# Optimization experiments

Measured on AMD Instinct MI355X. Metric: run time of the kernel, lower is better.

The kernel has to match this reference:

```python
import jax, jax.numpy as jnp
import numpy as np

TAU = 2.0       # LIF time constant
VTH = 1.0       # V_THRESHOLD
ALPHA = 2.0     # ATan surrogate alpha (spikingjelly default)
SCALE = 0.125

@jax.custom_vjp
def spike(x):
    # Heaviside spike with ATan surrogate gradient
    return (x >= 0.0).astype(x.dtype)

def _spike_fwd(x):
    return (x >= 0.0).astype(x.dtype), x

def _spike_bwd(x, g):
    sg = (ALPHA / 2.0) / (1.0 + (jnp.pi / 2.0 * ALPHA * x) ** 2)
    return (g * sg,)

spike.defvjp(_spike_fwd, _spike_bwd)

def lif(x_seq):
    # multi-step LIF: v += (x - v)/tau; spike; hard reset (v_reset=0, detach_reset)
    def step(v, x):
        v = v + (x - v) / TAU
        s = spike(v - VTH)
        v = v * (1.0 - jax.lax.stop_gradient(s))
        return v, s
    _, s = jax.lax.scan(step, jnp.zeros_like(x_seq[0]), x_seq)
    return s

def conn_lif(x_seq, y_seq):
    # connecting LIF: membrane charged by conv output + identity shortcut
    def step(v, xy):
        x, y = xy
        v = v + ((x + y) - v) / TAU
        s = spike(v - VTH)
        v = v * (1.0 - jax.lax.stop_gradient(s))
        return v, s
    _, s = jax.lax.scan(step, jnp.zeros_like(x_seq[0]), (x_seq, y_seq))
    return s

def conv1x1(x, W, b):
    # x: [T,B,C,N]; 1x1 Conv1d == channel GEMM
    return jnp.einsum('tbcn,oc->tbon', x, W) + b[None, None, :, None]

def setup_inputs() -> dict:
    key = jax.random.key(0)
    T, B, C, H, W = 4, 16, 512, 32, 32
    ks = jax.random.split(key, 5)
    wscale = 1.0 / np.sqrt(C)
    inp = {
        'x': jax.random.normal(ks[0], (T, B, C, H, W), jnp.float32),
        'Wq': jax.random.normal(ks[1], (C, C), jnp.float32) * wscale,
        'bq': jnp.zeros((C,), jnp.float32),
        'Wk': jax.random.normal(ks[2], (C, C), jnp.float32) * wscale,
        'bk': jnp.zeros((C,), jnp.float32),
        'Wv': jax.random.normal(ks[3], (C, C), jnp.float32) * wscale,
        'bv': jnp.zeros((C,), jnp.float32),
        'Wp': jax.random.normal(ks[4], (C, C), jnp.float32) * wscale,
        'bp': jnp.zeros((C,), jnp.float32),
        'num_heads': 8,
    }
    return inp

def reference(x, Wq, bq, Wk, bk, Wv, bv, Wp, bp, num_heads):
    T, B, C, H, W = x.shape
    N = H * W
    h = num_heads
    d = C // h
    qkv_x = x.reshape(T, B, C, N)

    def to_heads(s):  # [T,B,C,N] -> [T,B,h,N,d]
        return s.reshape(T, B, h, d, N).transpose(0, 1, 2, 4, 3)

    q = to_heads(lif(conv1x1(qkv_x, Wq, bq)))
    k = to_heads(lif(conv1x1(qkv_x, Wk, bk)))
    v = to_heads(lif(conv1x1(qkv_x, Wv, bv)))

    kv = jnp.einsum('tbhnd,tbhne->tbhde', k, v)            # K^T V: [T,B,h,d,d]
    out = jnp.einsum('tbhnd,tbhde->tbhne', q, kv) * SCALE  # Q @ (K^T V)
    out = out.transpose(0, 1, 2, 4, 3).reshape(T, B, C, N)
    out = lif(out)                                          # attn_sn
    out = conv1x1(out, Wp, bp).reshape(T, B, C, H, W)       # proj_reparam
    out = conn_lif(out, x)                                  # proj_sn(out, x)
    return out
```

## Files before the change

### kernel.cpp

```cpp
#include <hip/hip_runtime.h>

#define T_ 4
#define B_ 16
#define C_ 512
#define N_ 1024
#define H_ 8
#define D_ 64
#define SPK_ELEMS (33554432ull)

typedef _Float16 half8v __attribute__((ext_vector_type(8)));
typedef _Float16 half4v __attribute__((ext_vector_type(4)));
typedef float f32x4 __attribute__((ext_vector_type(4)));

#define KV_OFF_N  100663296ull
#define WB_OFF_N  109051904ull
#define XS_OFF_N  113246208ull

#define QKV_INV_SCALE (1.0f / 8388608.0f)
#define PROJ_INV_SCALE (1.0f / 4096.0f)

#define GLD16(gp, loff) \
  __builtin_amdgcn_global_load_lds( \
      (const __attribute__((address_space(1))) void*)(gp), \
      (__attribute__((address_space(3))) void*)(lds + (loff)), 16, 0, 0)

__global__ __launch_bounds__(256) void convert_w(
    const float* __restrict__ w0, const float* __restrict__ w1,
    const float* __restrict__ w2, const float* __restrict__ w3,
    _Float16* __restrict__ wb)
{
  int idx = blockIdx.x * 256 + threadIdx.x;
  int p = idx >> 18, rem = idx & 262143;
  const float* src = (p == 0) ? w0 : (p == 1) ? w1 : (p == 2) ? w2 : w3;
  float v = src[rem] * 4096.0f;
  _Float16 h1 = (_Float16)v;
  float r1 = v - (float)h1;
  _Float16 h2 = (_Float16)r1;
  size_t base = ((size_t)(p * 2)) << 18;
  wb[base + rem] = h1;
  wb[base + 262144 + rem] = h2;
}

__global__ __launch_bounds__(256) void convert_x(
    const float* __restrict__ x, _Float16* __restrict__ xs)
{
  __shared__ float tile[32][33];
  const int tb = blockIdx.z;
  const int c0 = blockIdx.y * 32, n0 = blockIdx.x * 32;
  const int tx = threadIdx.x, ty = threadIdx.y;
  const float* src = x + ((size_t)tb * C_ + c0) * N_ + n0;
#pragma unroll
  for (int k = 0; k < 4; ++k)
    tile[ty + 8 * k][tx] = src[(size_t)(ty + 8 * k) * N_ + tx];
  __syncthreads();
#pragma unroll
  for (int k = 0; k < 4; ++k) {
    int r = ty + 8 * k;
    float v = tile[tx][r] * 2048.0f;
    _Float16 h1 = (_Float16)v;
    float r1 = v - (float)h1;
    _Float16 h2 = (_Float16)r1;
    size_t o = ((size_t)tb * N_ + n0 + r) * C_ + c0 + tx;
    xs[o] = h1;
    xs[o + 33554432ull] = h2;
  }
}

__global__ __launch_bounds__(256) void qkv_mfma(
    const _Float16* __restrict__ wb, const _Float16* __restrict__ xs,
    const float* __restrict__ bq, const float* __restrict__ bk,
    const float* __restrict__ bv, unsigned char* __restrict__ spikes_base)
{
  __shared__ __align__(16) char lds[65536];
  const int tid = threadIdx.x;
  const int lane = tid & 63, wave = tid >> 6;
  const int ln15 = lane & 15, lq = lane >> 4;
  const int ot = blockIdx.x & 3, p = blockIdx.x >> 2;
  const int ntb = blockIdx.y, b = blockIdx.z;
  const int o0 = ot * 128, n0 = ntb * 32;

  const _Float16* gsrc[8];
#pragma unroll
  for (int i = 0; i < 8; ++i) {
    int u = i * 256 + tid;
    if (u < 1024) {
      int s = u >> 9, rem = u & 511;
      int row = rem >> 2, pc = rem & 3;
      int lc = pc ^ ((row >> 1) & 3);
      gsrc[i] = wb + (((size_t)(p * 2 + s)) << 18) + (size_t)(o0 + row) * C_ + lc * 8;
    } else {
      int v = u - 1024;
      int s = v >> 9, rem = v & 511;
      int t = rem >> 7, rem2 = rem & 127;
      int row = rem2 >> 2, pc = rem2 & 3;
      int lc = pc ^ ((row >> 1) & 3);
      gsrc[i] = xs + ((size_t)s * 33554432ull) +
                ((size_t)((t * B_ + b) * N_ + n0 + row)) * C_ + lc * 8;
    }
  }

  f32x4 acc[T_][2][2];
#pragma unroll
  for (int t = 0; t < T_; ++t)
#pragma unroll
    for (int mt = 0; mt < 2; ++mt)
#pragma unroll
      for (int nt = 0; nt < 2; ++nt)
        acc[t][mt][nt] = (f32x4){0.f, 0.f, 0.f, 0.f};

  int offA[2][2], offB[2][2];
#pragma unroll
  for (int s = 0; s < 2; ++s) {
#pragma unroll
    for (int mt = 0; mt < 2; ++mt) {
      int r = wave * 32 + mt * 16 + ln15;
      offA[s][mt] = s * 8192 + r * 64 + ((lq ^ ((r >> 1) & 3)) << 4);
    }
#pragma unroll
    for (int nt = 0; nt < 2; ++nt) {
      int n = nt * 16 + ln15;
      offB[s][nt] = 16384 + s * 8192 + n * 64 + ((lq ^ ((n >> 1) & 3)) << 4);
    }
  }

  auto compute = [&](int cur) {
    half8v wa[2][2];
#pragma unroll
    for (int s = 0; s < 2; ++s)
#pragma unroll
      for (int mt = 0; mt < 2; ++mt)
        wa[s][mt] = *(const half8v*)&lds[cur + offA[s][mt]];

    __builtin_amdgcn_s_setprio(1);
#pragma unroll
    for (int t = 0; t < T_; ++t) {
      half8v xb[2][2];
#pragma unroll
      for (int s = 0; s < 2; ++s)
#pragma unroll
        for (int nt = 0; nt < 2; ++nt)
          xb[s][nt] = *(const half8v*)&lds[cur + offB[s][nt] + t * 2048];
#pragma unroll
      for (int mt = 0; mt < 2; ++mt)
#pragma unroll
        for (int nt = 0; nt < 2; ++nt) {
          f32x4 a = acc[t][mt][nt];
          a = __builtin_amdgcn_mfma_f32_16x16x32_f16(wa[0][mt], xb[1][nt], a, 0, 0, 0);
          a = __builtin_amdgcn_mfma_f32_16x16x32_f16(wa[1][mt], xb[0][nt], a, 0, 0, 0);
          a = __builtin_amdgcn_mfma_f32_16x16x32_f16(wa[0][mt], xb[0][nt], a, 0, 0, 0);
          acc[t][mt][nt] = a;
        }
    }
    __builtin_amdgcn_s_setprio(0);
  };

#pragma unroll
  for (int i = 0; i < 8; ++i)
    GLD16(gsrc[i], i * 4096 + (tid & 192) * 16);
#pragma unroll
  for (int i = 0; i < 8; ++i) gsrc[i] += 32;

  for (int kk = 0; kk < 15; ++kk) {
    const int cur = (kk & 1) << 15;
    const int nxt = cur ^ 32768;
#pragma unroll
    for (int i = 0; i < 8; ++i)
      GLD16(gsrc[i], nxt + i * 4096 + (tid & 192) * 16);
#pragma unroll
    for (int i = 0; i < 8; ++i) gsrc[i] += 32;
    __builtin_amdgcn_sched_barrier(0);
    asm volatile("s_waitcnt vmcnt(8)" ::: "memory");
    __builtin_amdgcn_s_barrier();
    __builtin_amdgcn_sched_barrier(0);

    compute(cur);

    asm volatile("s_waitcnt lgkmcnt(0)" ::: "memory");
    __builtin_amdgcn_sched_barrier(0);
    __builtin_amdgcn_s_barrier();
  }
  asm volatile("s_waitcnt vmcnt(0)" ::: "memory");
  __builtin_amdgcn_s_barrier();
  __builtin_amdgcn_sched_barrier(0);
  compute(32768);

  const float* bias = (p == 0) ? bq : (p == 1) ? bk : bv;
  if (p == 0) {
    unsigned char* spq = spikes_base;
#pragma unroll
    for (int mt = 0; mt < 2; ++mt) {
      int obase = o0 + wave * 32 + mt * 16 + lq * 4;
      float b4[4] = {bias[obase], bias[obase + 1], bias[obase + 2], bias[obase + 3]};
#pragma unroll
      for (int nt = 0; nt < 2; ++nt) {
        int n = n0 + nt * 16 + ln15;
        float vm[4] = {0.f, 0.f, 0.f, 0.f};
#pragma unroll
        for (int t = 0; t < T_; ++t) {
          unsigned char sj[4];
#pragma unroll
          for (int r = 0; r < 4; ++r) {
            float y = acc[t][mt][nt][r] * QKV_INV_SCALE + b4[r];
            float v = vm[r] + (y - vm[r]) * 0.5f;
            bool s = (v >= 1.0f);
            sj[r] = s ? 1 : 0;
            vm[r] = s ? 0.f : v;
          }
          *(uchar4*)&spq[((size_t)(t * B_ + b) * N_ + n) * C_ + obase] =
              make_uchar4(sj[0], sj[1], sj[2], sj[3]);
        }
      }
    }
  } else {
    unsigned char* sp = spikes_base + (size_t)p * SPK_ELEMS;
#pragma unroll
    for (int mt = 0; mt < 2; ++mt)
#pragma unroll
      for (int r = 0; r < 4; ++r) {
        int o = o0 + wave * 32 + mt * 16 + lq * 4 + r;
        float bo = bias[o];
#pragma unroll
        for (int nt = 0; nt < 2; ++nt) {
          int n = n0 + nt * 16 + ln15;
          float vmem = 0.f;
#pragma unroll
          for (int t = 0; t < T_; ++t) {
            float y = acc[t][mt][nt][r] * QKV_INV_SCALE + bo;
            float v = vmem + (y - vmem) * 0.5f;
            bool s = (v >= 1.0f);
            sp[((size_t)(t * B_ + b) * C_ + o) * N_ + n] = s ? 1 : 0;
            vmem = s ? 0.f : v;
          }
        }
      }
  }
}

__global__ __launch_bounds__(256) void kv_f16(
    const unsigned char* __restrict__ sk, const unsigned char* __restrict__ sv,
    float* __restrict__ kvout)
{
  __shared__ _Float16 Kf[64 * 264];
  __shared__ _Float16 Vf[64 * 264];
  const int tid = threadIdx.x;
  const int lane = tid & 63, wave = tid >> 6;
  const int ln15 = lane & 15, lq = lane >> 4;
  const int h = blockIdx.x, b = blockIdx.y, t = blockIdx.z;

  const unsigned char* kb = sk + ((size_t)(t * B_ + b) * C_ + h * D_) * N_;
  const unsigned char* vb = sv + ((size_t)(t * B_ + b) * C_ + h * D_) * N_;

  f32x4 acc[4];
#pragma unroll
  for (int et = 0; et < 4; ++et) acc[et] = (f32x4){0.f, 0.f, 0.f, 0.f};

  const int row = tid >> 2, seg = (tid & 3) * 64;

  for (int nc = 0; nc < N_; nc += 256) {
    const unsigned char* kr = kb + (size_t)row * N_ + nc + seg;
    const unsigned char* vr = vb + (size_t)row * N_ + nc + seg;
#pragma unroll
    for (int j = 0; j < 16; ++j) {
      unsigned wk = *(const unsigned*)(kr + j * 4);
      unsigned lo = ((wk & 0xFFu) | ((wk & 0xFF00u) << 8)) * 0x3C00u;
      unsigned hi = (((wk >> 16) & 0xFFu) | ((wk >> 8) & 0xFF0000u)) * 0x3C00u;
      *(uint2*)&Kf[row * 264 + seg + j * 4] = make_uint2(lo, hi);
      unsigned wv = *(const unsigned*)(vr + j * 4);
      unsigned lo2 = ((wv & 0xFFu) | ((wv & 0xFF00u) << 8)) * 0x3C00u;
      unsigned hi2 = (((wv >> 16) & 0xFFu) | ((wv >> 8) & 0xFF0000u)) * 0x3C00u;
      *(uint2*)&Vf[row * 264 + seg + j * 4] = make_uint2(lo2, hi2);
    }
    __syncthreads();
#pragma unroll
    for (int ks = 0; ks < 8; ++ks) {
      half8v a = *(const half8v*)&Kf[(wave * 16 + ln15) * 264 + ks * 32 + lq * 8];
#pragma unroll
      for (int et = 0; et < 4; ++et) {
        half8v bf = *(const half8v*)&Vf[(et * 16 + ln15) * 264 + ks * 32 + lq * 8];
        acc[et] = __builtin_amdgcn_mfma_f32_16x16x32_f16(a, bf, acc[et], 0, 0, 0);
      }
    }
    __syncthreads();
  }

  float* o = kvout + ((size_t)(t * B_ + b) * H_ + h) * (D_ * D_);
#pragma unroll
  for (int et = 0; et < 4; ++et)
#pragma unroll
    for (int r = 0; r < 4; ++r) {
      int d = wave * 16 + lq * 4 + r;
      int e = et * 16 + ln15;
      o[d * D_ + e] = acc[et][r];
    }
}

__global__ __launch_bounds__(256) void attn_mfma(
    const unsigned char* __restrict__ sq2, const float* __restrict__ kv,
    unsigned short* __restrict__ sa)
{
  __shared__ _Float16 Qs[128 * 72];
  __shared__ _Float16 KVT[64 * 72];
  const int tid = threadIdx.x;
  const int lane = tid & 63, wave = tid >> 6;
  const int ln15 = lane & 15, lq = lane >> 4;
  const int n0 = blockIdx.x * 128;
  const int h = blockIdx.y, b = blockIdx.z;

  f32x4 vm[8];
#pragma unroll
  for (int nt = 0; nt < 8; ++nt) vm[nt] = (f32x4){0.f, 0.f, 0.f, 0.f};

  for (int t = 0; t < T_; ++t) {
    __syncthreads();
    const float* kvb = kv + ((size_t)(t * B_ + b) * H_ + h) * (D_ * D_);
#pragma unroll
    for (int l = 0; l < 16; ++l) {
      int idx = l * 256 + tid;
      int e = idx & 63, d = idx >> 6;
      KVT[e * 72 + d] = (_Float16)kvb[d * 64 + e];
    }
    const unsigned char* qb = sq2 + ((size_t)(t * B_ + b) * N_ + n0) * C_ + h * D_;
#pragma unroll
    for (int l = 0; l < 8; ++l) {
      int idx = l * 256 + tid;
      int n = idx >> 4, d4 = (idx & 15) * 4;
      uchar4 qu = *(const uchar4*)&qb[(size_t)n * C_ + d4];
      half4v hv;
      hv.x = qu.x ? (_Float16)1.0f : (_Float16)0.0f;
      hv.y = qu.y ? (_Float16)1.0f : (_Float16)0.0f;
      hv.z = qu.z ? (_Float16)1.0f : (_Float16)0.0f;
      hv.w = qu.w ? (_Float16)1.0f : (_Float16)0.0f;
      *(half4v*)&Qs[n * 72 + d4] = hv;
    }
    __syncthreads();

    half8v af[2];
#pragma unroll
    for (int kk = 0; kk < 2; ++kk)
      af[kk] = *(const half8v*)&KVT[(wave * 16 + ln15) * 72 + kk * 32 + lq * 8];

#pragma unroll
    for (int nt = 0; nt < 8; ++nt) {
      f32x4 a = (f32x4){0.f, 0.f, 0.f, 0.f};
#pragma unroll
      for (int kk = 0; kk < 2; ++kk) {
        half8v bf = *(const half8v*)&Qs[(nt * 16 + ln15) * 72 + kk * 32 + lq * 8];
        a = __builtin_amdgcn_mfma_f32_16x16x32_f16(af[kk], bf, a, 0, 0, 0);
      }
      unsigned short sj[4];
#pragma unroll
      for (int r = 0; r < 4; ++r) {
        float y = a[r] * 0.125f;
        float v = vm[nt][r] + (y - vm[nt][r]) * 0.5f;
        bool s = (v >= 1.0f);
        sj[r] = s ? 0x3C00 : 0;
        vm[nt][r] = s ? 0.f : v;
      }
      int n = n0 + nt * 16 + ln15;
      int c0 = h * D_ + wave * 16 + lq * 4;
      *(ushort4*)&sa[((size_t)(t * B_ + b) * N_ + n) * C_ + c0] =
          make_ushort4(sj[0], sj[1], sj[2], sj[3]);
    }
  }
}

__global__ __launch_bounds__(256) void proj_mfma(
    const _Float16* __restrict__ wb, const _Float16* __restrict__ sa,
    const float* __restrict__ bp, const float* __restrict__ x,
    float* __restrict__ out)
{
  __shared__ __align__(16) char lds[49152];
  const int tid = threadIdx.x;
  const int lane = tid & 63, wave = tid >> 6;
  const int ln15 = lane & 15, lq = lane >> 4;
  const int ot = blockIdx.x, ntb = blockIdx.y, b = blockIdx.z;
  const int o0 = ot * 128, n0 = ntb * 32;

  const _Float16* gsrc[6];
#pragma unroll
  for (int i = 0; i < 6; ++i) {
    int u = i * 256 + tid;
    if (u < 1024) {
      int s = u >> 9, rem = u & 511;
      int row = rem >> 2, pc = rem & 3;
      int lc = pc ^ ((row >> 1) & 3);
      gsrc[i] = wb + (((size_t)(3 * 2 + s)) << 18) + (size_t)(o0 + row) * C_ + lc * 8;
    } else {
      int v = u - 1024;
      int t = v >> 7, rem2 = v & 127;
      int row = rem2 >> 2, pc = rem2 & 3;
      int lc = pc ^ ((row >> 1) & 3);
      gsrc[i] = sa + ((size_t)((t * B_ + b) * N_ + n0 + row)) * C_ + lc * 8;
    }
  }

  f32x4 acc[T_][2][2];
#pragma unroll
  for (int t = 0; t < T_; ++t)
#pragma unroll
    for (int mt = 0; mt < 2; ++mt)
#pragma unroll
      for (int nt = 0; nt < 2; ++nt)
        acc[t][mt][nt] = (f32x4){0.f, 0.f, 0.f, 0.f};

  int offA[2][2], offB[2];
#pragma unroll
  for (int s = 0; s < 2; ++s)
#pragma unroll
    for (int mt = 0; mt < 2; ++mt) {
      int r = wave * 32 + mt * 16 + ln15;
      offA[s][mt] = s * 8192 + r * 64 + ((lq ^ ((r >> 1) & 3)) << 4);
    }
#pragma unroll
  for (int nt = 0; nt < 2; ++nt) {
    int n = nt * 16 + ln15;
    offB[nt] = 16384 + n * 64 + ((lq ^ ((n >> 1) & 3)) << 4);
  }

  auto compute = [&](int cur) {
    half8v wa[2][2];
#pragma unroll
    for (int s = 0; s < 2; ++s)
#pragma unroll
      for (int mt = 0; mt < 2; ++mt)
        wa[s][mt] = *(const half8v*)&lds[cur + offA[s][mt]];

    __builtin_amdgcn_s_setprio(1);
#pragma unroll
    for (int t = 0; t < T_; ++t) {
      half8v xb[2];
#pragma unroll
      for (int nt = 0; nt < 2; ++nt)
        xb[nt] = *(const half8v*)&lds[cur + offB[nt] + t * 2048];
#pragma unroll
      for (int mt = 0; mt < 2; ++mt)
#pragma unroll
        for (int nt = 0; nt < 2; ++nt) {
          f32x4 a = acc[t][mt][nt];
          a = __builtin_amdgcn_mfma_f32_16x16x32_f16(wa[1][mt], xb[nt], a, 0, 0, 0);
          a = __builtin_amdgcn_mfma_f32_16x16x32_f16(wa[0][mt], xb[nt], a, 0, 0, 0);
          acc[t][mt][nt] = a;
        }
    }
    __builtin_amdgcn_s_setprio(0);
  };

#pragma unroll
  for (int i = 0; i < 6; ++i)
    GLD16(gsrc[i], i * 4096 + (tid & 192) * 16);
#pragma unroll
  for (int i = 0; i < 6; ++i) gsrc[i] += 32;

  for (int kk = 0; kk < 15; ++kk) {
    const int cur = (kk & 1) * 24576;
    const int nxt = 24576 - cur;
#pragma unroll
    for (int i = 0; i < 6; ++i)
      GLD16(gsrc[i], nxt + i * 4096 + (tid & 192) * 16);
#pragma unroll
    for (int i = 0; i < 6; ++i) gsrc[i] += 32;
    __builtin_amdgcn_sched_barrier(0);
    asm volatile("s_waitcnt vmcnt(6)" ::: "memory");
    __builtin_amdgcn_s_barrier();
    __builtin_amdgcn_sched_barrier(0);

    compute(cur);

    asm volatile("s_waitcnt lgkmcnt(0)" ::: "memory");
    __builtin_amdgcn_sched_barrier(0);
    __builtin_amdgcn_s_barrier();
  }
  asm volatile("s_waitcnt vmcnt(0)" ::: "memory");
  __builtin_amdgcn_s_barrier();
  __builtin_amdgcn_sched_barrier(0);
  compute(24576);

#pragma unroll
  for (int mt = 0; mt < 2; ++mt)
#pragma unroll
    for (int r = 0; r < 4; ++r) {
      int o = o0 + wave * 32 + mt * 16 + lq * 4 + r;
      float bo = bp[o];
#pragma unroll
      for (int nt = 0; nt < 2; ++nt) {
        int n = n0 + nt * 16 + ln15;
        float vmem = 0.f;
#pragma unroll
        for (int t = 0; t < T_; ++t) {
          size_t base = ((size_t)(t * B_ + b) * C_ + o) * N_ + n;
          float xv = x[base];
          float pv = acc[t][mt][nt][r] * PROJ_INV_SCALE + bo;
          float v = vmem + ((pv + xv) - vmem) * 0.5f;
          bool s = (v >= 1.0f);
          out[base] = s ? 1.0f : 0.0f;
          vmem = s ? 0.f : v;
        }
      }
    }
}

extern "C" void kernel_launch(void* const* d_in, const int* in_sizes, int n_in,
                              void* d_out, int out_size, void* d_ws, size_t ws_size,
                              hipStream_t stream)
{
  const float* x  = (const float*)d_in[0];
  const float* Wq = (const float*)d_in[1];
  const float* bq = (const float*)d_in[2];
  const float* Wk = (const float*)d_in[3];
  const float* bk = (const float*)d_in[4];
  const float* Wv = (const float*)d_in[5];
  const float* bv = (const float*)d_in[6];
  const float* Wp = (const float*)d_in[7];
  const float* bp = (const float*)d_in[8];
  (void)in_sizes; (void)n_in; (void)out_size; (void)ws_size;

  unsigned char* ws = (unsigned char*)d_ws;
  unsigned char* sq = ws;
  unsigned char* sk = ws + SPK_ELEMS;
  unsigned char* sv = ws + 2 * SPK_ELEMS;
  float* kvbuf = (float*)(ws + KV_OFF_N);
  _Float16* wb = (_Float16*)(ws + WB_OFF_N);
  _Float16* xs = (_Float16*)(ws + XS_OFF_N);
  unsigned short* sa = (unsigned short*)xs;
  float* out = (float*)d_out;

  convert_w<<<4096, 256, 0, stream>>>(Wq, Wk, Wv, Wp, wb);
  convert_x<<<dim3(32, 16, 64), dim3(32, 8), 0, stream>>>(x, xs);
  qkv_mfma<<<dim3(12, 32, 16), 256, 0, stream>>>(wb, xs, bq, bk, bv, ws);
  kv_f16<<<dim3(8, 16, 4), 256, 0, stream>>>(sk, sv, kvbuf);
  attn_mfma<<<dim3(8, 8, 16), 256, 0, stream>>>(sq, kvbuf, sa);
  proj_mfma<<<dim3(4, 32, 16), 256, 0, stream>>>(wb, (const _Float16*)sa, bp, x, out);
}
```

Baseline: 790.0 us.

## Stream GEMM weights directly into double-buffered registers instead of staging through LDS

In both the QKV and projection GEMM kernels, the weight tiles are no longer copied into shared memory with global-to-LDS loads. Each wave now reads its own weight rows straight from global memory into a two-slot register buffer, prefetching the next K-slice while the current one is used. Only the activation tiles still go through LDS, which halves the QKV LDS footprint and cuts the projection's to a third, and the K loop is now fully unrolled. The aim is to remove LDS traffic and LDS reads for weights and allow more blocks per CU. The cost is more VGPRs and narrower, strided global loads that rely on L2 hits.

```diff
diff --git a/kernel.cpp b/kernel.cpp
--- a/kernel.cpp
+++ b/kernel.cpp
@@ -71,7 +71,7 @@
     const float* __restrict__ bq, const float* __restrict__ bk,
     const float* __restrict__ bv, unsigned char* __restrict__ spikes_base)
 {
-  __shared__ __align__(16) char lds[65536];
+  __shared__ __align__(16) char lds[32768];
   const int tid = threadIdx.x;
   const int lane = tid & 63, wave = tid >> 6;
   const int ln15 = lane & 15, lq = lane >> 4;
@@ -79,25 +79,26 @@
   const int ntb = blockIdx.y, b = blockIdx.z;
   const int o0 = ot * 128, n0 = ntb * 32;
 
-  const _Float16* gsrc[8];
-#pragma unroll
-  for (int i = 0; i < 8; ++i) {
+  const _Float16* gsrc[4];
+#pragma unroll
+  for (int i = 0; i < 4; ++i) {
     int u = i * 256 + tid;
-    if (u < 1024) {
-      int s = u >> 9, rem = u & 511;
-      int row = rem >> 2, pc = rem & 3;
-      int lc = pc ^ ((row >> 1) & 3);
-      gsrc[i] = wb + (((size_t)(p * 2 + s)) << 18) + (size_t)(o0 + row) * C_ + lc * 8;
-    } else {
-      int v = u - 1024;
-      int s = v >> 9, rem = v & 511;
-      int t = rem >> 7, rem2 = rem & 127;
-      int row = rem2 >> 2, pc = rem2 & 3;
-      int lc = pc ^ ((row >> 1) & 3);
-      gsrc[i] = xs + ((size_t)s * 33554432ull) +
-                ((size_t)((t * B_ + b) * N_ + n0 + row)) * C_ + lc * 8;
-    }
-  }
+    int s = u >> 9, rem = u & 511;
+    int t = rem >> 7, rem2 = rem & 127;
+    int row = rem2 >> 2, pc = rem2 & 3;
+    int lc = pc ^ ((row >> 1) & 3);
+    gsrc[i] = xs + ((size_t)s * 33554432ull) +
+              ((size_t)((t * B_ + b) * N_ + n0 + row)) * C_ + lc * 8;
+  }
+
+  const _Float16* wsrc[2][2];
+#pragma unroll
+  for (int s = 0; s < 2; ++s)
+#pragma unroll
+    for (int mt = 0; mt < 2; ++mt) {
+      int r = o0 + wave * 32 + mt * 16 + ln15;
+      wsrc[s][mt] = wb + (((size_t)(p * 2 + s)) << 18) + (size_t)r * C_ + lq * 8;
+    }
 
   f32x4 acc[T_][2][2];
 #pragma unroll
@@ -108,29 +109,18 @@
       for (int nt = 0; nt < 2; ++nt)
         acc[t][mt][nt] = (f32x4){0.f, 0.f, 0.f, 0.f};
 
-  int offA[2][2], offB[2][2];
-#pragma unroll
-  for (int s = 0; s < 2; ++s) {
-#pragma unroll
-    for (int mt = 0; mt < 2; ++mt) {
-      int r = wave * 32 + mt * 16 + ln15;
-      offA[s][mt] = s * 8192 + r * 64 + ((lq ^ ((r >> 1) & 3)) << 4);
-    }
+  int offB[2][2];
+#pragma unroll
+  for (int s = 0; s < 2; ++s)
 #pragma unroll
     for (int nt = 0; nt < 2; ++nt) {
       int n = nt * 16 + ln15;
-      offB[s][nt] = 16384 + s * 8192 + n * 64 + ((lq ^ ((n >> 1) & 3)) << 4);
-    }
-  }
-
-  auto compute = [&](int cur) {
-    half8v wa[2][2];
-#pragma unroll
-    for (int s = 0; s < 2; ++s)
-#pragma unroll
-      for (int mt = 0; mt < 2; ++mt)
-        wa[s][mt] = *(const half8v*)&lds[cur + offA[s][mt]];
-
+      offB[s][nt] = s * 8192 + n * 64 + ((lq ^ ((n >> 1) & 3)) << 4);
+    }
+
+  half8v wreg[2][2][2];
+
+  auto compute = [&](int cur, int pc_) {
     __builtin_amdgcn_s_setprio(1);
 #pragma unroll
     for (int t = 0; t < T_; ++t) {
@@ -145,9 +135,9 @@
 #pragma unroll
         for (int nt = 0; nt < 2; ++nt) {
           f32x4 a = acc[t][mt][nt];
-          a = __builtin_amdgcn_mfma_f32_16x16x32_f16(wa[0][mt], xb[1][nt], a, 0, 0, 0);
-          a = __builtin_amdgcn_mfma_f32_16x16x32_f16(wa[1][mt], xb[0][nt], a, 0, 0, 0);
-          a = __builtin_amdgcn_mfma_f32_16x16x32_f16(wa[0][mt], xb[0][nt], a, 0, 0, 0);
+          a = __builtin_amdgcn_mfma_f32_16x16x32_f16(wreg[pc_][0][mt], xb[1][nt], a, 0, 0, 0);
+          a = __builtin_amdgcn_mfma_f32_16x16x32_f16(wreg[pc_][1][mt], xb[0][nt], a, 0, 0, 0);
+          a = __builtin_amdgcn_mfma_f32_16x16x32_f16(wreg[pc_][0][mt], xb[0][nt], a, 0, 0, 0);
           acc[t][mt][nt] = a;
         }
     }
@@ -155,25 +145,37 @@
   };
 
 #pragma unroll
-  for (int i = 0; i < 8; ++i)
+  for (int i = 0; i < 4; ++i)
     GLD16(gsrc[i], i * 4096 + (tid & 192) * 16);
 #pragma unroll
-  for (int i = 0; i < 8; ++i) gsrc[i] += 32;
-
+  for (int i = 0; i < 4; ++i) gsrc[i] += 32;
+#pragma unroll
+  for (int s = 0; s < 2; ++s)
+#pragma unroll
+    for (int mt = 0; mt < 2; ++mt)
+      wreg[0][s][mt] = *(const half8v*)(wsrc[s][mt]);
+
+#pragma unroll
   for (int kk = 0; kk < 15; ++kk) {
-    const int cur = (kk & 1) << 15;
-    const int nxt = cur ^ 32768;
-#pragma unroll
-    for (int i = 0; i < 8; ++i)
+    const int cur = (kk & 1) * 16384;
+    const int nxt = 16384 - cur;
+    const int pc_ = kk & 1, pn_ = pc_ ^ 1;
+#pragma unroll
+    for (int i = 0; i < 4; ++i)
       GLD16(gsrc[i], nxt + i * 4096 + (tid & 192) * 16);
 #pragma unroll
-    for (int i = 0; i < 8; ++i) gsrc[i] += 32;
+    for (int i = 0; i < 4; ++i) gsrc[i] += 32;
+#pragma unroll
+    for (int s = 0; s < 2; ++s)
+#pragma unroll
+      for (int mt = 0; mt < 2; ++mt)
+        wreg[pn_][s][mt] = *(const half8v*)(wsrc[s][mt] + (kk + 1) * 32);
     __builtin_amdgcn_sched_barrier(0);
     asm volatile("s_waitcnt vmcnt(8)" ::: "memory");
     __builtin_amdgcn_s_barrier();
     __builtin_amdgcn_sched_barrier(0);
 
-    compute(cur);
+    compute(cur, pc_);
 
     asm volatile("s_waitcnt lgkmcnt(0)" ::: "memory");
     __builtin_amdgcn_sched_barrier(0);
@@ -182,7 +184,7 @@
   asm volatile("s_waitcnt vmcnt(0)" ::: "memory");
   __builtin_amdgcn_s_barrier();
   __builtin_amdgcn_sched_barrier(0);
-  compute(32768);
+  compute(16384, 1);
 
   const float* bias = (p == 0) ? bq : (p == 1) ? bk : bv;
   if (p == 0) {
@@ -369,30 +371,31 @@
     const float* __restrict__ bp, const float* __restrict__ x,
     float* __restrict__ out)
 {
-  __shared__ __align__(16) char lds[49152];
+  __shared__ __align__(16) char lds[16384];
   const int tid = threadIdx.x;
   const int lane = tid & 63, wave = tid >> 6;
   const int ln15 = lane & 15, lq = lane >> 4;
   const int ot = blockIdx.x, ntb = blockIdx.y, b = blockIdx.z;
   const int o0 = ot * 128, n0 = ntb * 32;
 
-  const _Float16* gsrc[6];
-#pragma unroll
-  for (int i = 0; i < 6; ++i) {
+  const _Float16* gsrc[2];
+#pragma unroll
+  for (int i = 0; i < 2; ++i) {
     int u = i * 256 + tid;
-    if (u < 1024) {
-      int s = u >> 9, rem = u & 511;
-      int row = rem >> 2, pc = rem & 3;
-      int lc = pc ^ ((row >> 1) & 3);
-      gsrc[i] = wb + (((size_t)(3 * 2 + s)) << 18) + (size_t)(o0 + row) * C_ + lc * 8;
-    } else {
-      int v = u - 1024;
-      int t = v >> 7, rem2 = v & 127;
-      int row = rem2 >> 2, pc = rem2 & 3;
-      int lc = pc ^ ((row >> 1) & 3);
-      gsrc[i] = sa + ((size_t)((t * B_ + b) * N_ + n0 + row)) * C_ + lc * 8;
-    }
-  }
+    int t = u >> 7, rem2 = u & 127;
+    int row = rem2 >> 2, pc = rem2 & 3;
+    int lc = pc ^ ((row >> 1) & 3);
+    gsrc[i] = sa + ((size_t)((t * B_ + b) * N_ + n0 + row)) * C_ + lc * 8;
+  }
+
+  const _Float16* wsrc[2][2];
+#pragma unroll
+  for (int s = 0; s < 2; ++s)
+#pragma unroll
+    for (int mt = 0; mt < 2; ++mt) {
+      int r = o0 + wave * 32 + mt * 16 + ln15;
+      wsrc[s][mt] = wb + (((size_t)(3 * 2 + s)) << 18) + (size_t)r * C_ + lq * 8;
+    }
 
   f32x4 acc[T_][2][2];
 #pragma unroll
@@ -403,28 +406,16 @@
       for (int nt = 0; nt < 2; ++nt)
         acc[t][mt][nt] = (f32x4){0.f, 0.f, 0.f, 0.f};
 
-  int offA[2][2], offB[2];
-#pragma unroll
-  for (int s = 0; s < 2; ++s)
-#pragma unroll
-    for (int mt = 0; mt < 2; ++mt) {
-      int r = wave * 32 + mt * 16 + ln15;
-      offA[s][mt] = s * 8192 + r * 64 + ((lq ^ ((r >> 1) & 3)) << 4);
-    }
+  int offB[2];
 #pragma unroll
   for (int nt = 0; nt < 2; ++nt) {
     int n = nt * 16 + ln15;
-    offB[nt] = 16384 + n * 64 + ((lq ^ ((n >> 1) & 3)) << 4);
-  }
-
-  auto compute = [&](int cur) {
-    half8v wa[2][2];
-#pragma unroll
-    for (int s = 0; s < 2; ++s)
-#pragma unroll
-      for (int mt = 0; mt < 2; ++mt)
-        wa[s][mt] = *(const half8v*)&lds[cur + offA[s][mt]];
-
+    offB[nt] = n * 64 + ((lq ^ ((n >> 1) & 3)) << 4);
+  }
+
+  half8v wreg[2][2][2];
+
+  auto compute = [&](int cur, int pc_) {
     __builtin_amdgcn_s_setprio(1);
 #pragma unroll
     for (int t = 0; t < T_; ++t) {
@@ -437,8 +428,8 @@
 #pragma unroll
         for (int nt = 0; nt < 2; ++nt) {
           f32x4 a = acc[t][mt][nt];
-          a = __builtin_amdgcn_mfma_f32_16x16x32_f16(wa[1][mt], xb[nt], a, 0, 0, 0);
-          a = __builtin_amdgcn_mfma_f32_16x16x32_f16(wa[0][mt], xb[nt], a, 0, 0, 0);
+          a = __builtin_amdgcn_mfma_f32_16x16x32_f16(wreg[pc_][1][mt], xb[nt], a, 0, 0, 0);
+          a = __builtin_amdgcn_mfma_f32_16x16x32_f16(wreg[pc_][0][mt], xb[nt], a, 0, 0, 0);
           acc[t][mt][nt] = a;
         }
     }
@@ -446,25 +437,37 @@
   };
 
 #pragma unroll
-  for (int i = 0; i < 6; ++i)
+  for (int i = 0; i < 2; ++i)
     GLD16(gsrc[i], i * 4096 + (tid & 192) * 16);
 #pragma unroll
-  for (int i = 0; i < 6; ++i) gsrc[i] += 32;
-
+  for (int i = 0; i < 2; ++i) gsrc[i] += 32;
+#pragma unroll
+  for (int s = 0; s < 2; ++s)
+#pragma unroll
+    for (int mt = 0; mt < 2; ++mt)
+      wreg[0][s][mt] = *(const half8v*)(wsrc[s][mt]);
+
+#pragma unroll
   for (int kk = 0; kk < 15; ++kk) {
-    const int cur = (kk & 1) * 24576;
-    const int nxt = 24576 - cur;
-#pragma unroll
-    for (int i = 0; i < 6; ++i)
+    const int cur = (kk & 1) * 8192;
+    const int nxt = 8192 - cur;
+    const int pc_ = kk & 1, pn_ = pc_ ^ 1;
+#pragma unroll
+    for (int i = 0; i < 2; ++i)
       GLD16(gsrc[i], nxt + i * 4096 + (tid & 192) * 16);
 #pragma unroll
-    for (int i = 0; i < 6; ++i) gsrc[i] += 32;
+    for (int i = 0; i < 2; ++i) gsrc[i] += 32;
+#pragma unroll
+    for (int s = 0; s < 2; ++s)
+#pragma unroll
+      for (int mt = 0; mt < 2; ++mt)
+        wreg[pn_][s][mt] = *(const half8v*)(wsrc[s][mt] + (kk + 1) * 32);
     __builtin_amdgcn_sched_barrier(0);
     asm volatile("s_waitcnt vmcnt(6)" ::: "memory");
     __builtin_amdgcn_s_barrier();
     __builtin_amdgcn_sched_barrier(0);
 
-    compute(cur);
+    compute(cur, pc_);
 
     asm volatile("s_waitcnt lgkmcnt(0)" ::: "memory");
     __builtin_amdgcn_sched_barrier(0);
@@ -473,7 +476,7 @@
   asm volatile("s_waitcnt vmcnt(0)" ::: "memory");
   __builtin_amdgcn_s_barrier();
   __builtin_amdgcn_sched_barrier(0);
-  compute(24576);
+  compute(8192, 1);
 
 #pragma unroll
   for (int mt = 0; mt < 2; ++mt)
```

New measurement: 809.3 us. 2.4% more time.

## Triple-buffer activation tiles in QKV GEMM to deepen prefetch pipeline

Applied to the files above, without the earlier changes.

Splits the QKV GEMM's LDS staging into separate weight and activation buffers. Weights stay double-buffered, while activation tiles get three buffers and are prefetched two K-steps ahead, with the wait counts adjusted to match. The aim is to hide more global-memory latency for the streamed activation tiles. In exchange, LDS per block grows from 64KB to 80KB, which may reduce the number of blocks that fit on a CU, and the K loop is now fully unrolled.

```diff
diff --git a/kernel.cpp b/kernel.cpp
--- a/kernel.cpp
+++ b/kernel.cpp
@@ -71,7 +71,7 @@
     const float* __restrict__ bq, const float* __restrict__ bk,
     const float* __restrict__ bv, unsigned char* __restrict__ spikes_base)
 {
-  __shared__ __align__(16) char lds[65536];
+  __shared__ __align__(16) char lds[81920];
   const int tid = threadIdx.x;
   const int lane = tid & 63, wave = tid >> 6;
   const int ln15 = lane & 15, lq = lane >> 4;
@@ -79,24 +79,28 @@
   const int ntb = blockIdx.y, b = blockIdx.z;
   const int o0 = ot * 128, n0 = ntb * 32;
 
-  const _Float16* gsrc[8];
-#pragma unroll
-  for (int i = 0; i < 8; ++i) {
+#define WB_(k) (((k) & 1) * 16384)
+#define XB_(k) (32768 + ((k) % 3) * 16384)
+
+  const _Float16* gw[4];
+#pragma unroll
+  for (int i = 0; i < 4; ++i) {
     int u = i * 256 + tid;
-    if (u < 1024) {
-      int s = u >> 9, rem = u & 511;
-      int row = rem >> 2, pc = rem & 3;
-      int lc = pc ^ ((row >> 1) & 3);
-      gsrc[i] = wb + (((size_t)(p * 2 + s)) << 18) + (size_t)(o0 + row) * C_ + lc * 8;
-    } else {
-      int v = u - 1024;
-      int s = v >> 9, rem = v & 511;
-      int t = rem >> 7, rem2 = rem & 127;
-      int row = rem2 >> 2, pc = rem2 & 3;
-      int lc = pc ^ ((row >> 1) & 3);
-      gsrc[i] = xs + ((size_t)s * 33554432ull) +
-                ((size_t)((t * B_ + b) * N_ + n0 + row)) * C_ + lc * 8;
-    }
+    int s = u >> 9, rem = u & 511;
+    int row = rem >> 2, pc = rem & 3;
+    int lc = pc ^ ((row >> 1) & 3);
+    gw[i] = wb + (((size_t)(p * 2 + s)) << 18) + (size_t)(o0 + row) * C_ + lc * 8;
+  }
+  const _Float16* gx[4];
+#pragma unroll
+  for (int i = 0; i < 4; ++i) {
+    int v = i * 256 + tid;
+    int s = v >> 9, rem = v & 511;
+    int t = rem >> 7, rem2 = rem & 127;
+    int row = rem2 >> 2, pc = rem2 & 3;
+    int lc = pc ^ ((row >> 1) & 3);
+    gx[i] = xs + ((size_t)s * 33554432ull) +
+            ((size_t)((t * B_ + b) * N_ + n0 + row)) * C_ + lc * 8;
   }
 
   f32x4 acc[T_][2][2];
@@ -119,17 +123,17 @@
 #pragma unroll
     for (int nt = 0; nt < 2; ++nt) {
       int n = nt * 16 + ln15;
-      offB[s][nt] = 16384 + s * 8192 + n * 64 + ((lq ^ ((n >> 1) & 3)) << 4);
-    }
-  }
-
-  auto compute = [&](int cur) {
+      offB[s][nt] = s * 8192 + n * 64 + ((lq ^ ((n >> 1) & 3)) << 4);
+    }
+  }
+
+  auto compute = [&](int wbase, int xbase) {
     half8v wa[2][2];
 #pragma unroll
     for (int s = 0; s < 2; ++s)
 #pragma unroll
       for (int mt = 0; mt < 2; ++mt)
-        wa[s][mt] = *(const half8v*)&lds[cur + offA[s][mt]];
+        wa[s][mt] = *(const half8v*)&lds[wbase + offA[s][mt]];
 
     __builtin_amdgcn_s_setprio(1);
 #pragma unroll
@@ -139,7 +143,7 @@
       for (int s = 0; s < 2; ++s)
 #pragma unroll
         for (int nt = 0; nt < 2; ++nt)
-          xb[s][nt] = *(const half8v*)&lds[cur + offB[s][nt] + t * 2048];
+          xb[s][nt] = *(const half8v*)&lds[xbase + offB[s][nt] + t * 2048];
 #pragma unroll
       for (int mt = 0; mt < 2; ++mt)
 #pragma unroll
@@ -155,25 +159,42 @@
   };
 
 #pragma unroll
-  for (int i = 0; i < 8; ++i)
-    GLD16(gsrc[i], i * 4096 + (tid & 192) * 16);
-#pragma unroll
-  for (int i = 0; i < 8; ++i) gsrc[i] += 32;
-
+  for (int i = 0; i < 4; ++i)
+    GLD16(gx[i], XB_(0) + i * 4096 + (tid & 192) * 16);
+#pragma unroll
+  for (int i = 0; i < 4; ++i) gx[i] += 32;
+#pragma unroll
+  for (int i = 0; i < 4; ++i)
+    GLD16(gw[i], WB_(0) + i * 4096 + (tid & 192) * 16);
+#pragma unroll
+  for (int i = 0; i < 4; ++i) gw[i] += 32;
+#pragma unroll
+  for (int i = 0; i < 4; ++i)
+    GLD16(gx[i], XB_(1) + i * 4096 + (tid & 192) * 16);
+#pragma unroll
+  for (int i = 0; i < 4; ++i) gx[i] += 32;
+
+#pragma unroll
   for (int kk = 0; kk < 15; ++kk) {
-    const int cur = (kk & 1) << 15;
-    const int nxt = cur ^ 32768;
-#pragma unroll
-    for (int i = 0; i < 8; ++i)
-      GLD16(gsrc[i], nxt + i * 4096 + (tid & 192) * 16);
-#pragma unroll
-    for (int i = 0; i < 8; ++i) gsrc[i] += 32;
+#pragma unroll
+    for (int i = 0; i < 4; ++i)
+      GLD16(gw[i], WB_(kk + 1) + i * 4096 + (tid & 192) * 16);
+#pragma unroll
+    for (int i = 0; i < 4; ++i) gw[i] += 32;
+    if (kk < 14) {
+#pragma unroll
+      for (int i = 0; i < 4; ++i)
+        GLD16(gx[i], XB_(kk + 2) + i * 4096 + (tid & 192) * 16);
+#pragma unroll
+      for (int i = 0; i < 4; ++i) gx[i] += 32;
+    }
     __builtin_amdgcn_sched_barrier(0);
-    asm volatile("s_waitcnt vmcnt(8)" ::: "memory");
+    if (kk < 14) asm volatile("s_waitcnt vmcnt(12)" ::: "memory");
+    else         asm volatile("s_waitcnt vmcnt(8)"  ::: "memory");
     __builtin_amdgcn_s_barrier();
     __builtin_amdgcn_sched_barrier(0);
 
-    compute(cur);
+    compute(WB_(kk), XB_(kk));
 
     asm volatile("s_waitcnt lgkmcnt(0)" ::: "memory");
     __builtin_amdgcn_sched_barrier(0);
@@ -182,7 +203,10 @@
   asm volatile("s_waitcnt vmcnt(0)" ::: "memory");
   __builtin_amdgcn_s_barrier();
   __builtin_amdgcn_sched_barrier(0);
-  compute(32768);
+  compute(WB_(15), XB_(15));
+
+#undef WB_
+#undef XB_
 
   const float* bias = (p == 0) ? bq : (p == 1) ? bk : bv;
   if (p == 0) {
```

Result: faster. 759.3 us (-3.9%).
